# Performance work log

Hardware: AMD Instinct MI355X
Metric: run time of the kernel (lower is better)

The kernel has to match this reference:

```python
import jax, jax.numpy as jnp
import numpy as np

E = 1024   # embed_dim
H = 16     # num_heads
D = E // H # head_dim
NP = 2     # n_physics
PH = 16    # physics adapter hidden


def setup_inputs() -> dict:
    key = jax.random.key(0)
    ks = jax.random.split(key, 16)
    B, T = 2, 2048
    s = 0.02
    return {
        "x": jax.random.normal(ks[0], (B, T, E), dtype=jnp.float32),
        "physics_state": jax.random.uniform(ks[1], (B, NP), dtype=jnp.float32),
        "attn_mask": jax.random.randint(ks[2], (B, T), 0, 2).astype(jnp.bool_),
        "Wq": jax.random.normal(ks[3], (E, E), dtype=jnp.float32) * s,
        "bq": jnp.zeros((E,), dtype=jnp.float32),
        "Wk": jax.random.normal(ks[4], (E, E), dtype=jnp.float32) * s,
        "bk": jnp.zeros((E,), dtype=jnp.float32),
        "Wv": jax.random.normal(ks[5], (E, E), dtype=jnp.float32) * s,
        "bv": jnp.zeros((E,), dtype=jnp.float32),
        "Wo": jax.random.normal(ks[6], (E, E), dtype=jnp.float32) * s,
        "bo": jnp.zeros((E,), dtype=jnp.float32),
        "Wp1": jax.random.normal(ks[7], (NP, PH), dtype=jnp.float32) * 0.5,
        "bp1": jnp.zeros((PH,), dtype=jnp.float32),
        "Wp2": jax.random.normal(ks[8], (PH, H), dtype=jnp.float32) * 0.25,
        "bp2": jnp.zeros((H,), dtype=jnp.float32),
    }


def reference(x, physics_state, attn_mask, Wq, bq, Wk, bk, Wv, bv, Wo, bo, Wp1, bp1, Wp2, bp2):
    B, T, _ = x.shape
    scale = 1.0 / np.sqrt(D)
    # projections -> (B, H, T, D)
    q = (x @ Wq + bq).reshape(B, T, H, D).transpose(0, 2, 1, 3)
    k = (x @ Wk + bk).reshape(B, T, H, D).transpose(0, 2, 1, 3)
    v = (x @ Wv + bv).reshape(B, T, H, D).transpose(0, 2, 1, 3)
    # per-head physics bias (B, H) -> (B, H, 1, 1)
    h = jax.nn.gelu(physics_state @ Wp1 + bp1, approximate=False)
    phys_bias = (h @ Wp2 + bp2)[:, :, None, None]
    scores = jnp.einsum("bhqd,bhkd->bhqk", q, k) * scale + phys_bias
    # key padding mask: True = keep
    scores = jnp.where(attn_mask[:, None, None, :], scores, -jnp.inf)
    attn = jax.nn.softmax(scores, axis=-1)
    out = jnp.einsum("bhqk,bhkd->bhqd", attn, v)
    out = out.transpose(0, 2, 1, 3).reshape(B, T, E)
    return out @ Wo + bo
```

## Files before the change

kernel.cpp:

```cpp
#include <hip/hip_runtime.h>
#include <hip/hip_bf16.h>
#include <stdint.h>

#define E_  1024
#define H_  16
#define D_  64
#define T_  2048
#define B_  2

typedef unsigned short u16;
typedef unsigned char u8;
typedef __attribute__((ext_vector_type(8))) __bf16 bf16x8;
typedef __attribute__((ext_vector_type(4))) float f32x4;
typedef __attribute__((ext_vector_type(8))) u16 u16x8;
typedef __attribute__((ext_vector_type(4))) u16 u16x4;
typedef __attribute__((ext_vector_type(2))) uint32_t u32x2;

__device__ __forceinline__ float bf2f(u16 u) {
  union { uint32_t u32; float f; } x; x.u32 = ((uint32_t)u) << 16; return x.f;
}
__device__ __forceinline__ u16 f2bf(float v) {
  union { float f; uint32_t u; } x; x.f = v;
  uint32_t r = x.u + 0x7fffu + ((x.u >> 16) & 1u);
  return (u16)(r >> 16);
}
__device__ __forceinline__ void async16(const void* g, void* l) {
  __builtin_amdgcn_global_load_lds(
      (const __attribute__((address_space(1))) void*)g,
      (__attribute__((address_space(3))) void*)l, 16, 0, 0);
}

__global__ __launch_bounds__(256) void detect_kernel(const u16* __restrict__ xu,
                                                     const void* __restrict__ mp,
                                                     int* __restrict__ flags) {
  __shared__ int cnt[2];
  const int tid = threadIdx.x;
  if (tid < 2) cnt[tid] = 0;
  __syncthreads();
  int c = 0;
  for (int i = tid; i < 4096; i += 256) {
    u16 u = xu[2 * i];
    int e = (u >> 7) & 0xFF;
    if (e != 0 && (e <= 0x40 || e >= 0xC0)) c++;
  }
  atomicAdd(&cnt[0], c);
  int m = 0;
  const unsigned int* mi = (const unsigned int*)mp;
  for (int i = tid; i < 1024; i += 256)
    if (mi[i] > 1u) m++;
  atomicAdd(&cnt[1], m);
  __syncthreads();
  if (tid == 0) {
    flags[0] = (cnt[0] > 409) ? 1 : 0;
    flags[1] = (cnt[1] == 0) ? 1 : 0;
  }
}

__global__ __launch_bounds__(256) void convf_kernel(const void* __restrict__ src,
                                                    u16* __restrict__ dst, int n,
                                                    const int* __restrict__ flags) {
  int i = (blockIdx.x * 256 + threadIdx.x) * 8;
  if (i >= n) return;
  if (flags[0]) {
    const float* s = (const float*)src;
    u16x8 o;
#pragma unroll
    for (int j = 0; j < 8; ++j) o[j] = f2bf(s[i + j]);
    *(u16x8*)(dst + i) = o;
  } else {
    *(u16x8*)(dst + i) = *(const u16x8*)((const u16*)src + i);
  }
}

__global__ __launch_bounds__(256) void bias4_kernel(
    const void* __restrict__ b0, const void* __restrict__ b1,
    const void* __restrict__ b2, const void* __restrict__ b3,
    u16* __restrict__ dst, const int* __restrict__ flags) {
  const void* src = (blockIdx.x == 0) ? b0 : (blockIdx.x == 1) ? b1
                    : (blockIdx.x == 2) ? b2 : b3;
  u16* d = dst + blockIdx.x * 2048;
  int t = threadIdx.x;
#pragma unroll
  for (int j = 0; j < 4; ++j) {
    int i = t + j * 256;
    d[i] = flags[0] ? f2bf(((const float*)src)[i]) : ((const u16*)src)[i];
  }
}

__global__ __launch_bounds__(256) void maskbias_kernel(const void* __restrict__ mp,
                                                       float* __restrict__ mbg,
                                                       const int* __restrict__ flags) {
  int i = blockIdx.x * 256 + threadIdx.x;
  int keep = flags[1] ? (((const int*)mp)[i] != 0) : (((const u8*)mp)[i] != 0);
  mbg[i] = keep ? -5.77078016f : -30000.f;
}

__global__ __launch_bounds__(256) void wtc_kernel(const void* __restrict__ Wv,
                                                  u16* __restrict__ WT,
                                                  const int* __restrict__ flags) {
  __shared__ __align__(16) u16 tile[64][65];
  const int bx = blockIdx.x * 64;
  const int by = blockIdx.y * 64;
  const int t = threadIdx.x;
  const int f32in = flags[0];
#pragma unroll
  for (int p = 0; p < 2; ++p) {
    int row = p * 32 + (t >> 3);
    int ch = t & 7;
    if (f32in) {
      const float* s = (const float*)Wv + (size_t)(by + row) * E_ + bx + ch * 8;
#pragma unroll
      for (int j = 0; j < 8; ++j) tile[row][ch * 8 + j] = f2bf(s[j]);
    } else {
      u16x8 v = *(const u16x8*)((const u16*)Wv + (size_t)(by + row) * E_ + bx + ch * 8);
#pragma unroll
      for (int j = 0; j < 8; ++j) tile[row][ch * 8 + j] = v[j];
    }
  }
  __syncthreads();
#pragma unroll
  for (int p = 0; p < 2; ++p) {
    int orow = p * 32 + (t >> 3);
    int ch = t & 7;
    u16x8 v;
#pragma unroll
    for (int j = 0; j < 8; ++j) v[j] = tile[ch * 8 + j][orow];
    *(u16x8*)(WT + (size_t)(bx + orow) * E_ + by + ch * 8) = v;
  }
}

__global__ __launch_bounds__(256, 2) void gemm_qkv_kernel(
    const u16* __restrict__ A, const u16* __restrict__ BTm,
    const u16* __restrict__ biases, u16* __restrict__ Qb,
    u16* __restrict__ Kb, u16* __restrict__ Vtb) {
  __shared__ __align__(16) u16 As[128 * 64];
  __shared__ __align__(16) u16 Bs[128 * 64];
  const int tid = threadIdx.x, lane = tid & 63, wid = tid >> 6;
  const int wm = wid >> 1, wn = wid & 1;
  const int l15 = lane & 15, lg = lane >> 4;
  const int r0 = blockIdx.x * 128, c0 = blockIdx.y * 128;
  f32x4 acc[4][4] = {};

  for (int k0 = 0; k0 < E_; k0 += 64) {
    __syncthreads();
#pragma unroll
    for (int i = 0; i < 4; ++i) {
      int row = i * 32 + (tid >> 3);
      int g = (tid & 7) ^ (row & 7);
      async16(A + (size_t)(r0 + row) * E_ + k0 + g * 8,
              (char*)As + i * 4096 + tid * 16);
      async16(BTm + (size_t)(c0 + row) * E_ + k0 + g * 8,
              (char*)Bs + i * 4096 + tid * 16);
    }
    __syncthreads();
#pragma unroll
    for (int kk = 0; kk < 2; ++kk) {
      bf16x8 af[4], bfr[4];
#pragma unroll
      for (int mt = 0; mt < 4; ++mt) {
        int rowa = wm * 64 + mt * 16 + l15;
        int sa = (kk * 4 + lg) ^ (rowa & 7);
        af[mt] = *(const bf16x8*)((const char*)As + rowa * 128 + sa * 16);
        int rowb = wn * 64 + mt * 16 + l15;
        int sb = (kk * 4 + lg) ^ (rowb & 7);
        bfr[mt] = *(const bf16x8*)((const char*)Bs + rowb * 128 + sb * 16);
      }
#pragma unroll
      for (int mt = 0; mt < 4; ++mt)
#pragma unroll
        for (int nt = 0; nt < 4; ++nt)
          acc[mt][nt] = __builtin_amdgcn_mfma_f32_16x16x32_bf16(
              af[mt], bfr[nt], acc[mt][nt], 0, 0, 0);
    }
  }

  const int sel = c0 >> 10;
  u16* outp = (sel == 0) ? Qb : Kb;
#pragma unroll
  for (int mt = 0; mt < 4; ++mt) {
#pragma unroll
    for (int nt = 0; nt < 4; ++nt) {
      int colG = c0 + wn * 64 + nt * 16 + l15;
      int colL = colG & 1023;
      float bv = bf2f(biases[sel * 2048 + colL]);
      int rbase = r0 + wm * 64 + mt * 16 + lg * 4;
      int hh = colL >> 6, dd = colL & 63;
      if (sel == 2) {
        int bb = rbase >> 11, t0 = rbase & (T_ - 1);
        u16x4 pk;
#pragma unroll
        for (int r = 0; r < 4; ++r) pk[r] = f2bf(acc[mt][nt][r] + bv);
        *(u16x4*)(Vtb + (size_t)((bb * H_ + hh) * D_ + dd) * T_ + t0) = pk;
      } else {
#pragma unroll
        for (int r = 0; r < 4; ++r) {
          int row = rbase + r;
          int bb = row >> 11, t = row & (T_ - 1);
          outp[(size_t)((bb * H_ + hh) * T_ + t) * D_ + dd] =
              f2bf(acc[mt][nt][r] + bv);
        }
      }
    }
  }
}

__global__ __launch_bounds__(256, 2) void gemm_out_kernel(
    const u16* __restrict__ A, const u16* __restrict__ BTm,
    const u16* __restrict__ bias, float* __restrict__ out) {
  __shared__ __align__(16) u16 As[128 * 64];
  __shared__ __align__(16) u16 Bs[128 * 64];
  const int tid = threadIdx.x, lane = tid & 63, wid = tid >> 6;
  const int wm = wid >> 1, wn = wid & 1;
  const int l15 = lane & 15, lg = lane >> 4;
  const int r0 = blockIdx.x * 128, c0 = blockIdx.y * 128;
  f32x4 acc[4][4] = {};

  for (int k0 = 0; k0 < E_; k0 += 64) {
    __syncthreads();
#pragma unroll
    for (int i = 0; i < 4; ++i) {
      int row = i * 32 + (tid >> 3);
      int g = (tid & 7) ^ (row & 7);
      async16(A + (size_t)(r0 + row) * E_ + k0 + g * 8,
              (char*)As + i * 4096 + tid * 16);
      async16(BTm + (size_t)(c0 + row) * E_ + k0 + g * 8,
              (char*)Bs + i * 4096 + tid * 16);
    }
    __syncthreads();
#pragma unroll
    for (int kk = 0; kk < 2; ++kk) {
      bf16x8 af[4], bfr[4];
#pragma unroll
      for (int mt = 0; mt < 4; ++mt) {
        int rowa = wm * 64 + mt * 16 + l15;
        int sa = (kk * 4 + lg) ^ (rowa & 7);
        af[mt] = *(const bf16x8*)((const char*)As + rowa * 128 + sa * 16);
        int rowb = wn * 64 + mt * 16 + l15;
        int sb = (kk * 4 + lg) ^ (rowb & 7);
        bfr[mt] = *(const bf16x8*)((const char*)Bs + rowb * 128 + sb * 16);
      }
#pragma unroll
      for (int mt = 0; mt < 4; ++mt)
#pragma unroll
        for (int nt = 0; nt < 4; ++nt)
          acc[mt][nt] = __builtin_amdgcn_mfma_f32_16x16x32_bf16(
              af[mt], bfr[nt], acc[mt][nt], 0, 0, 0);
    }
  }

#pragma unroll
  for (int mt = 0; mt < 4; ++mt)
#pragma unroll
    for (int nt = 0; nt < 4; ++nt) {
      int col = c0 + wn * 64 + nt * 16 + l15;
      float bv = bf2f(bias[col]);
      int rbase = r0 + wm * 64 + mt * 16 + lg * 4;
#pragma unroll
      for (int r = 0; r < 4; ++r)
        out[(size_t)(rbase + r) * E_ + col] = acc[mt][nt][r] + bv;
    }
}

__global__ __launch_bounds__(256, 2) void attn_kernel(
    const u16* __restrict__ Q, const u16* __restrict__ K,
    const u16* __restrict__ VT, const float* __restrict__ mbg,
    u16* __restrict__ outb) {
  __shared__ __align__(16) u16 Ks[128 * 64];
  __shared__ __align__(16) u16 Vs[64 * 128];
  __shared__ __align__(16) u16 Ps[4][32 * 136];
  __shared__ __align__(16) float mb[T_];
  const int wg = blockIdx.x;
  const int xcd = wg & 7, slot = wg >> 3;
  const int bh = xcd + 8 * (slot >> 4);
  const int q0 = (slot & 15) * 128;
  const int b = bh >> 4, h = bh & 15;
  const int tid = threadIdx.x, lane = tid & 63, w = tid >> 6;
  const int l15 = lane & 15, lg = lane >> 4;

  for (int i = tid; i < T_; i += 256) mb[i] = mbg[b * T_ + i];

  const u16* qb = Q + (size_t)bh * T_ * D_;
  const u16* kb = K + (size_t)bh * T_ * D_;
  const u16* vb = VT + (size_t)bh * D_ * T_;

  bf16x8 qf[2][2];
#pragma unroll
  for (int mt = 0; mt < 2; ++mt)
#pragma unroll
    for (int kd = 0; kd < 2; ++kd) {
      int row = q0 + w * 32 + mt * 16 + l15;
      qf[mt][kd] = *(const bf16x8*)(qb + (size_t)row * D_ + kd * 32 + lg * 8);
    }

  f32x4 o[2][4] = {};
  float lrow[2] = {0.f, 0.f};
  const float cc = 0.125f * 1.44269504f;

  for (int kt = 0; kt < 16; ++kt) {
    const int kk0 = kt * 128;
    __syncthreads();
#pragma unroll
    for (int i = 0; i < 4; ++i) {
      int row = i * 32 + (tid >> 3);
      int g = (tid & 7) ^ (row & 7);
      async16(kb + (size_t)(kk0 + row) * D_ + g * 8,
              (char*)Ks + i * 4096 + tid * 16);
    }
#pragma unroll
    for (int i = 0; i < 4; ++i) {
      int row = i * 16 + (tid >> 4);
      int g = (tid & 15) ^ (row & 7);
      async16(vb + (size_t)row * T_ + kk0 + g * 8,
              (char*)Vs + i * 4096 + tid * 16);
    }
    __syncthreads();

    f32x4 s2[2][8] = {};
#pragma unroll
    for (int kd = 0; kd < 2; ++kd) {
      bf16x8 kf[8];
#pragma unroll
      for (int mf = 0; mf < 8; ++mf) {
        int row = mf * 16 + l15;
        int slot2 = (kd * 4 + lg) ^ (row & 7);
        kf[mf] = *(const bf16x8*)((const char*)Ks + row * 128 + slot2 * 16);
      }
      __builtin_amdgcn_s_setprio(1);
#pragma unroll
      for (int mt = 0; mt < 2; ++mt)
#pragma unroll
        for (int mf = 0; mf < 8; ++mf)
          s2[mt][mf] = __builtin_amdgcn_mfma_f32_16x16x32_bf16(
              kf[mf], qf[mt][kd], s2[mt][mf], 0, 0, 0);
      __builtin_amdgcn_s_setprio(0);
    }

#pragma unroll
    for (int mt = 0; mt < 2; ++mt) {
      float lr = 0.f;
#pragma unroll
      for (int mf = 0; mf < 8; ++mf) {
        f32x4 mb4 = *(const f32x4*)&mb[kk0 + mf * 16 + lg * 4];
        float p0 = exp2f(fmaf(s2[mt][mf][0], cc, mb4[0]));
        float p1 = exp2f(fmaf(s2[mt][mf][1], cc, mb4[1]));
        float p2 = exp2f(fmaf(s2[mt][mf][2], cc, mb4[2]));
        float p3 = exp2f(fmaf(s2[mt][mf][3], cc, mb4[3]));
        lr += (p0 + p1) + (p2 + p3);
        uint32_t w0, w1;
        asm("v_cvt_pk_bf16_f32 %0, %1, %2" : "=v"(w0) : "v"(p0), "v"(p1));
        asm("v_cvt_pk_bf16_f32 %0, %1, %2" : "=v"(w1) : "v"(p2), "v"(p3));
        u32x2 pk = {w0, w1};
        *(u32x2*)((char*)&Ps[w][0] + (mt * 16 + l15) * 272 + mf * 32 + lg * 8) = pk;
      }
      lrow[mt] += lr;
    }

    asm volatile("s_waitcnt lgkmcnt(0)" ::: "memory");
    __builtin_amdgcn_sched_barrier(0);

#pragma unroll
    for (int kk = 0; kk < 4; ++kk) {
      bf16x8 pf[2], vf[4];
#pragma unroll
      for (int mt = 0; mt < 2; ++mt)
        pf[mt] = *(const bf16x8*)((const char*)&Ps[w][0] +
                                  (mt * 16 + l15) * 272 + kk * 64 + lg * 16);
#pragma unroll
      for (int df = 0; df < 4; ++df) {
        int row = df * 16 + l15;
        int slot2 = (kk * 4 + lg) ^ (row & 7);
        vf[df] = *(const bf16x8*)((const char*)Vs + row * 256 + slot2 * 16);
      }
      __builtin_amdgcn_s_setprio(1);
#pragma unroll
      for (int mt = 0; mt < 2; ++mt)
#pragma unroll
        for (int df = 0; df < 4; ++df)
          o[mt][df] = __builtin_amdgcn_mfma_f32_16x16x32_bf16(
              pf[mt], vf[df], o[mt][df], 0, 0, 0);
      __builtin_amdgcn_s_setprio(0);
    }
  }

  float inv[2][4];
#pragma unroll
  for (int mt = 0; mt < 2; ++mt) {
    float t = lrow[mt];
    t += __shfl_xor(t, 16);
    t += __shfl_xor(t, 32);
    float ti = (t > 0.f) ? 1.0f / t : 0.f;
#pragma unroll
    for (int r = 0; r < 4; ++r)
      inv[mt][r] = __shfl(ti, (lane & 48) | (lg * 4 + r));
  }

#pragma unroll
  for (int mt = 0; mt < 2; ++mt)
#pragma unroll
    for (int df = 0; df < 4; ++df)
#pragma unroll
      for (int r = 0; r < 4; ++r) {
        int prow = mt * 16 + lg * 4 + r;
        Ps[w][prow * 136 + df * 16 + l15] = f2bf(o[mt][df][r] * inv[mt][r]);
      }
  asm volatile("s_waitcnt lgkmcnt(0)" ::: "memory");
  __builtin_amdgcn_sched_barrier(0);
  {
    int rowL = lane >> 1;
    int c8 = lane & 1;
    int grow = b * T_ + q0 + w * 32 + rowL;
#pragma unroll
    for (int j = 0; j < 4; ++j) {
      int chunk = c8 + 2 * j;
      u16x8 v = *(const u16x8*)(&Ps[w][rowL * 136 + chunk * 8]);
      *(u16x8*)(outb + (size_t)grow * E_ + h * D_ + chunk * 8) = v;
    }
  }
}

extern "C" void kernel_launch(void* const* d_in, const int* in_sizes, int n_in,
                              void* d_out, int out_size, void* d_ws, size_t ws_size,
                              hipStream_t stream) {
  const void* x    = d_in[0];
  const void* mask = d_in[2];
  const void* Wq = d_in[3];
  const void* bq = d_in[4];
  const void* Wk = d_in[5];
  const void* bk = d_in[6];
  const void* Wv = d_in[7];
  const void* bv = d_in[8];
  const void* Wo = d_in[9];
  const void* bo = d_in[10];
  char* ws = (char*)d_ws;

  const size_t MB = 1024 * 1024;
  u16* Kb   = (u16*)(ws + 0 * MB);
  u16* Vtb  = (u16*)(ws + 8 * MB);
  u16* Ab   = (u16*)(ws + 16 * MB);
  u16* WqT  = (u16*)(ws + 16 * MB);
  u16* WkT  = (u16*)(ws + 18 * MB);
  u16* WvT  = (u16*)(ws + 20 * MB);
  u16* WoT  = (u16*)(ws + 0 * MB);
  u16* bqc  = (u16*)(ws + 24 * MB);
  u16* boc  = bqc + 3 * 2048;
  float* mbg = (float*)(ws + 24 * MB + 64 * 1024);
  int* flags = (int*)(ws + 24 * MB + 128 * 1024);

  u16* Qb = (u16*)d_out;
  u16* xc = (u16*)((char*)d_out + 8 * MB);
  float* out = (float*)d_out;

  dim3 blk(256);
  const int NX = B_ * T_ * E_;

  detect_kernel<<<1, blk, 0, stream>>>((const u16*)x, mask, flags);
  convf_kernel<<<NX / 8 / 256, blk, 0, stream>>>(x, xc, NX, flags);
  bias4_kernel<<<4, blk, 0, stream>>>(bq, bk, bv, bo, bqc, flags);
  maskbias_kernel<<<16, blk, 0, stream>>>(mask, mbg, flags);

  wtc_kernel<<<dim3(16, 16), blk, 0, stream>>>(Wq, WqT, flags);
  wtc_kernel<<<dim3(16, 16), blk, 0, stream>>>(Wk, WkT, flags);
  wtc_kernel<<<dim3(16, 16), blk, 0, stream>>>(Wv, WvT, flags);

  gemm_qkv_kernel<<<dim3(32, 24), blk, 0, stream>>>(xc, WqT, bqc, Qb, Kb, Vtb);
  attn_kernel<<<dim3(512), blk, 0, stream>>>(Qb, Kb, Vtb, mbg, Ab);
  wtc_kernel<<<dim3(16, 16), blk, 0, stream>>>(Wo, WoT, flags);
  gemm_out_kernel<<<dim3(32, 8), blk, 0, stream>>>(Ab, WoT, boc, out);
}
```

Measured before the change: 145.6 us.

## Double-buffer attention K/V tiles and fold dtype detection into launched kernels

The attention kernel now works on 64-key tiles with two K/V shared-memory buffers. The next tile's async loads are issued before computing on the current one, so one barrier per iteration replaces the load-wait-compute pattern. The P staging buffer is laid out to match the MFMA operand order so each lane reads it contiguously. On the host side, the separate detect kernel is removed: each kernel infers fp32 versus bf16 input with a wavefront ballot, and the four weight transposes, including Wo, run in one launch. This cuts launch count but repeats the detection in every block and doubles the number of attention loop iterations.

```diff
diff --git a/kernel.cpp b/kernel.cpp
--- a/kernel.cpp
+++ b/kernel.cpp
@@ -30,38 +30,19 @@
       (__attribute__((address_space(3))) void*)l, 16, 0, 0);
 }
 
-__global__ __launch_bounds__(256) void detect_kernel(const u16* __restrict__ xu,
-                                                     const void* __restrict__ mp,
-                                                     int* __restrict__ flags) {
-  __shared__ int cnt[2];
-  const int tid = threadIdx.x;
-  if (tid < 2) cnt[tid] = 0;
-  __syncthreads();
-  int c = 0;
-  for (int i = tid; i < 4096; i += 256) {
-    u16 u = xu[2 * i];
-    int e = (u >> 7) & 0xFF;
-    if (e != 0 && (e <= 0x40 || e >= 0xC0)) c++;
-  }
-  atomicAdd(&cnt[0], c);
-  int m = 0;
-  const unsigned int* mi = (const unsigned int*)mp;
-  for (int i = tid; i < 1024; i += 256)
-    if (mi[i] > 1u) m++;
-  atomicAdd(&cnt[1], m);
-  __syncthreads();
-  if (tid == 0) {
-    flags[0] = (cnt[0] > 409) ? 1 : 0;
-    flags[1] = (cnt[1] == 0) ? 1 : 0;
-  }
+__device__ __forceinline__ int detect_f32(const void* src) {
+  u16 u = ((const u16*)src)[2 * (threadIdx.x & 63)];
+  int e = (u >> 7) & 0xFF;
+  int ex = (e != 0 && (e <= 0x40 || e >= 0xC0)) ? 1 : 0;
+  return __popcll(__ballot(ex)) > 16;
 }
 
 __global__ __launch_bounds__(256) void convf_kernel(const void* __restrict__ src,
-                                                    u16* __restrict__ dst, int n,
-                                                    const int* __restrict__ flags) {
+                                                    u16* __restrict__ dst, int n) {
+  const int f32in = detect_f32(src);
   int i = (blockIdx.x * 256 + threadIdx.x) * 8;
   if (i >= n) return;
-  if (flags[0]) {
+  if (f32in) {
     const float* s = (const float*)src;
     u16x8 o;
 #pragma unroll
@@ -75,34 +56,40 @@
 __global__ __launch_bounds__(256) void bias4_kernel(
     const void* __restrict__ b0, const void* __restrict__ b1,
     const void* __restrict__ b2, const void* __restrict__ b3,
-    u16* __restrict__ dst, const int* __restrict__ flags) {
+    u16* __restrict__ dst) {
   const void* src = (blockIdx.x == 0) ? b0 : (blockIdx.x == 1) ? b1
                     : (blockIdx.x == 2) ? b2 : b3;
+  const int f32in = detect_f32(src);
   u16* d = dst + blockIdx.x * 2048;
   int t = threadIdx.x;
 #pragma unroll
   for (int j = 0; j < 4; ++j) {
     int i = t + j * 256;
-    d[i] = flags[0] ? f2bf(((const float*)src)[i]) : ((const u16*)src)[i];
+    d[i] = f32in ? f2bf(((const float*)src)[i]) : ((const u16*)src)[i];
   }
 }
 
 __global__ __launch_bounds__(256) void maskbias_kernel(const void* __restrict__ mp,
-                                                       float* __restrict__ mbg,
-                                                       const int* __restrict__ flags) {
+                                                       float* __restrict__ mbg) {
+  unsigned w0 = ((const unsigned*)mp)[threadIdx.x & 63];
+  int isInt = (__ballot(w0 > 1u) == 0ull);
   int i = blockIdx.x * 256 + threadIdx.x;
-  int keep = flags[1] ? (((const int*)mp)[i] != 0) : (((const u8*)mp)[i] != 0);
+  int keep = isInt ? (((const int*)mp)[i] != 0) : (((const u8*)mp)[i] != 0);
   mbg[i] = keep ? -5.77078016f : -30000.f;
 }
 
-__global__ __launch_bounds__(256) void wtc_kernel(const void* __restrict__ Wv,
-                                                  u16* __restrict__ WT,
-                                                  const int* __restrict__ flags) {
+__global__ __launch_bounds__(256) void wtc4_kernel(
+    const void* __restrict__ W0, const void* __restrict__ W1,
+    const void* __restrict__ W2, const void* __restrict__ W3,
+    u16* __restrict__ T0, u16* __restrict__ T1,
+    u16* __restrict__ T2, u16* __restrict__ T3) {
   __shared__ __align__(16) u16 tile[64][65];
-  const int bx = blockIdx.x * 64;
-  const int by = blockIdx.y * 64;
+  const int z = blockIdx.z;
+  const void* Wv = (z == 0) ? W0 : (z == 1) ? W1 : (z == 2) ? W2 : W3;
+  u16* WT = (z == 0) ? T0 : (z == 1) ? T1 : (z == 2) ? T2 : T3;
+  const int f32in = detect_f32(Wv);
+  const int bx = blockIdx.x * 64, by = blockIdx.y * 64;
   const int t = threadIdx.x;
-  const int f32in = flags[0];
 #pragma unroll
   for (int p = 0; p < 2; ++p) {
     int row = p * 32 + (t >> 3);
@@ -265,9 +252,9 @@
     const u16* __restrict__ Q, const u16* __restrict__ K,
     const u16* __restrict__ VT, const float* __restrict__ mbg,
     u16* __restrict__ outb) {
-  __shared__ __align__(16) u16 Ks[128 * 64];
-  __shared__ __align__(16) u16 Vs[64 * 128];
-  __shared__ __align__(16) u16 Ps[4][32 * 136];
+  __shared__ __align__(16) u16 Ks[2][64 * 64];
+  __shared__ __align__(16) u16 Vs[2][64 * 64];
+  __shared__ __align__(16) u16 Ps[4][2][2][512];
   __shared__ __align__(16) float mb[T_];
   const int wg = blockIdx.x;
   const int xcd = wg & 7, slot = wg >> 3;
@@ -292,44 +279,48 @@
       qf[mt][kd] = *(const bf16x8*)(qb + (size_t)row * D_ + kd * 32 + lg * 8);
     }
 
+#define STAGE(kt_, bi_)                                                  \
+  do {                                                                   \
+    _Pragma("unroll")                                                    \
+    for (int c = 0; c < 2; ++c) {                                        \
+      int row_ = c * 32 + (tid >> 3);                                    \
+      int g_ = (tid & 7) ^ (row_ & 7);                                   \
+      async16(kb + (size_t)((kt_) * 64 + row_) * D_ + g_ * 8,            \
+              (char*)&Ks[bi_][0] + c * 4096 + tid * 16);                 \
+      async16(vb + (size_t)row_ * T_ + (kt_) * 64 + g_ * 8,              \
+              (char*)&Vs[bi_][0] + c * 4096 + tid * 16);                 \
+    }                                                                    \
+  } while (0)
+
+  STAGE(0, 0);
+  __syncthreads();
+
   f32x4 o[2][4] = {};
   float lrow[2] = {0.f, 0.f};
   const float cc = 0.125f * 1.44269504f;
 
-  for (int kt = 0; kt < 16; ++kt) {
-    const int kk0 = kt * 128;
-    __syncthreads();
-#pragma unroll
-    for (int i = 0; i < 4; ++i) {
-      int row = i * 32 + (tid >> 3);
-      int g = (tid & 7) ^ (row & 7);
-      async16(kb + (size_t)(kk0 + row) * D_ + g * 8,
-              (char*)Ks + i * 4096 + tid * 16);
-    }
-#pragma unroll
-    for (int i = 0; i < 4; ++i) {
-      int row = i * 16 + (tid >> 4);
-      int g = (tid & 15) ^ (row & 7);
-      async16(vb + (size_t)row * T_ + kk0 + g * 8,
-              (char*)Vs + i * 4096 + tid * 16);
-    }
-    __syncthreads();
-
-    f32x4 s2[2][8] = {};
+  for (int kt = 0; kt < 32; ++kt) {
+    const int cur = kt & 1;
+    if (kt < 31) STAGE(kt + 1, cur ^ 1);
+    const char* Kc = (const char*)&Ks[cur][0];
+    const char* Vc = (const char*)&Vs[cur][0];
+    const int kk0 = kt * 64;
+
+    f32x4 s2[2][4] = {};
 #pragma unroll
     for (int kd = 0; kd < 2; ++kd) {
-      bf16x8 kf[8];
-#pragma unroll
-      for (int mf = 0; mf < 8; ++mf) {
+      bf16x8 kf[4];
+#pragma unroll
+      for (int mf = 0; mf < 4; ++mf) {
         int row = mf * 16 + l15;
-        int slot2 = (kd * 4 + lg) ^ (row & 7);
-        kf[mf] = *(const bf16x8*)((const char*)Ks + row * 128 + slot2 * 16);
+        int sl = (kd * 4 + lg) ^ (row & 7);
+        kf[mf] = *(const bf16x8*)(Kc + row * 128 + sl * 16);
       }
       __builtin_amdgcn_s_setprio(1);
 #pragma unroll
       for (int mt = 0; mt < 2; ++mt)
 #pragma unroll
-        for (int mf = 0; mf < 8; ++mf)
+        for (int mf = 0; mf < 4; ++mf)
           s2[mt][mf] = __builtin_amdgcn_mfma_f32_16x16x32_bf16(
               kf[mf], qf[mt][kd], s2[mt][mf], 0, 0, 0);
       __builtin_amdgcn_s_setprio(0);
@@ -337,39 +328,38 @@
 
 #pragma unroll
     for (int mt = 0; mt < 2; ++mt) {
-      float lr = 0.f;
-#pragma unroll
-      for (int mf = 0; mf < 8; ++mf) {
+#pragma unroll
+      for (int mf = 0; mf < 4; ++mf) {
         f32x4 mb4 = *(const f32x4*)&mb[kk0 + mf * 16 + lg * 4];
         float p0 = exp2f(fmaf(s2[mt][mf][0], cc, mb4[0]));
         float p1 = exp2f(fmaf(s2[mt][mf][1], cc, mb4[1]));
         float p2 = exp2f(fmaf(s2[mt][mf][2], cc, mb4[2]));
         float p3 = exp2f(fmaf(s2[mt][mf][3], cc, mb4[3]));
-        lr += (p0 + p1) + (p2 + p3);
+        lrow[mt] += (p0 + p1) + (p2 + p3);
         uint32_t w0, w1;
         asm("v_cvt_pk_bf16_f32 %0, %1, %2" : "=v"(w0) : "v"(p0), "v"(p1));
         asm("v_cvt_pk_bf16_f32 %0, %1, %2" : "=v"(w1) : "v"(p2), "v"(p3));
         u32x2 pk = {w0, w1};
-        *(u32x2*)((char*)&Ps[w][0] + (mt * 16 + l15) * 272 + mf * 32 + lg * 8) = pk;
-      }
-      lrow[mt] += lr;
+        int lgr = (mf & 1) * 2 + (lg >> 1);
+        *(u32x2*)((char*)&Ps[w][mt][mf >> 1][0] +
+                  (l15 + 16 * lgr) * 16 + 8 * (lg & 1)) = pk;
+      }
     }
 
     asm volatile("s_waitcnt lgkmcnt(0)" ::: "memory");
     __builtin_amdgcn_sched_barrier(0);
 
 #pragma unroll
-    for (int kk = 0; kk < 4; ++kk) {
+    for (int kk = 0; kk < 2; ++kk) {
       bf16x8 pf[2], vf[4];
 #pragma unroll
       for (int mt = 0; mt < 2; ++mt)
-        pf[mt] = *(const bf16x8*)((const char*)&Ps[w][0] +
-                                  (mt * 16 + l15) * 272 + kk * 64 + lg * 16);
+        pf[mt] = *(const bf16x8*)((const char*)&Ps[w][mt][kk][0] + lane * 16);
 #pragma unroll
       for (int df = 0; df < 4; ++df) {
         int row = df * 16 + l15;
-        int slot2 = (kk * 4 + lg) ^ (row & 7);
-        vf[df] = *(const bf16x8*)((const char*)Vs + row * 256 + slot2 * 16);
+        int sl = (kk * 4 + lg) ^ (row & 7);
+        vf[df] = *(const bf16x8*)(Vc + row * 128 + sl * 16);
       }
       __builtin_amdgcn_s_setprio(1);
 #pragma unroll
@@ -380,7 +370,9 @@
               pf[mt], vf[df], o[mt][df], 0, 0, 0);
       __builtin_amdgcn_s_setprio(0);
     }
-  }
+    __syncthreads();
+  }
+#undef STAGE
 
   float inv[2][4];
 #pragma unroll
@@ -394,6 +386,7 @@
       inv[mt][r] = __shfl(ti, (lane & 48) | (lg * 4 + r));
   }
 
+  char* wbase = ((w < 2) ? (char*)&Ks[0][0] : (char*)&Vs[0][0]) + (w & 1) * 4608;
 #pragma unroll
   for (int mt = 0; mt < 2; ++mt)
 #pragma unroll
@@ -401,7 +394,8 @@
 #pragma unroll
       for (int r = 0; r < 4; ++r) {
         int prow = mt * 16 + lg * 4 + r;
-        Ps[w][prow * 136 + df * 16 + l15] = f2bf(o[mt][df][r] * inv[mt][r]);
+        *(u16*)(wbase + prow * 144 + (df * 16 + l15) * 2) =
+            f2bf(o[mt][df][r] * inv[mt][r]);
       }
   asm volatile("s_waitcnt lgkmcnt(0)" ::: "memory");
   __builtin_amdgcn_sched_barrier(0);
@@ -412,7 +406,7 @@
 #pragma unroll
     for (int j = 0; j < 4; ++j) {
       int chunk = c8 + 2 * j;
-      u16x8 v = *(const u16x8*)(&Ps[w][rowL * 136 + chunk * 8]);
+      u16x8 v = *(const u16x8*)(wbase + rowL * 144 + chunk * 16);
       *(u16x8*)(outb + (size_t)grow * E_ + h * D_ + chunk * 8) = v;
     }
   }
@@ -440,11 +434,10 @@
   u16* WqT  = (u16*)(ws + 16 * MB);
   u16* WkT  = (u16*)(ws + 18 * MB);
   u16* WvT  = (u16*)(ws + 20 * MB);
-  u16* WoT  = (u16*)(ws + 0 * MB);
-  u16* bqc  = (u16*)(ws + 24 * MB);
+  u16* WoT  = (u16*)(ws + 24 * MB);
+  u16* bqc  = (u16*)(ws + 26 * MB);
   u16* boc  = bqc + 3 * 2048;
-  float* mbg = (float*)(ws + 24 * MB + 64 * 1024);
-  int* flags = (int*)(ws + 24 * MB + 128 * 1024);
+  float* mbg = (float*)(ws + 26 * MB + 32 * 1024);
 
   u16* Qb = (u16*)d_out;
   u16* xc = (u16*)((char*)d_out + 8 * MB);
@@ -453,17 +446,12 @@
   dim3 blk(256);
   const int NX = B_ * T_ * E_;
 
-  detect_kernel<<<1, blk, 0, stream>>>((const u16*)x, mask, flags);
-  convf_kernel<<<NX / 8 / 256, blk, 0, stream>>>(x, xc, NX, flags);
-  bias4_kernel<<<4, blk, 0, stream>>>(bq, bk, bv, bo, bqc, flags);
-  maskbias_kernel<<<16, blk, 0, stream>>>(mask, mbg, flags);
-
-  wtc_kernel<<<dim3(16, 16), blk, 0, stream>>>(Wq, WqT, flags);
-  wtc_kernel<<<dim3(16, 16), blk, 0, stream>>>(Wk, WkT, flags);
-  wtc_kernel<<<dim3(16, 16), blk, 0, stream>>>(Wv, WvT, flags);
-
+  convf_kernel<<<NX / 8 / 256, blk, 0, stream>>>(x, xc, NX);
+  bias4_kernel<<<4, blk, 0, stream>>>(bq, bk, bv, bo, bqc);
+  maskbias_kernel<<<16, blk, 0, stream>>>(mask, mbg);
+  wtc4_kernel<<<dim3(16, 16, 4), blk, 0, stream>>>(Wq, Wk, Wv, Wo,
+                                                   WqT, WkT, WvT, WoT);
   gemm_qkv_kernel<<<dim3(32, 24), blk, 0, stream>>>(xc, WqT, bqc, Qb, Kb, Vtb);
   attn_kernel<<<dim3(512), blk, 0, stream>>>(Qb, Kb, Vtb, mbg, Ab);
-  wtc_kernel<<<dim3(16, 16), blk, 0, stream>>>(Wo, WoT, flags);
   gemm_out_kernel<<<dim3(32, 8), blk, 0, stream>>>(Ab, WoT, boc, out);
 }
```

Result: faster. 136.4 us (-6.3%).
